# Kernel optimization log

Hardware: AMD Instinct MI355X
Metric: run time of the kernel (lower is better)

The kernel has to match this reference:

```python
import jax, jax.numpy as jnp
import numpy as np

B, DZ, DY, DX = 2, 200, 200, 100   # batch, voxel grid
N = 200000                          # active input voxels
C_IN, C_MID, C_OUT = 16, 64, 32
K = 27                              # 3x3x3 kernel offsets
EPS = 1e-5


def _pad_per_k(kid, a_in, a_out, pad_in, pad_out):
    # pack ragged per-offset pair lists into dense [K, Pmax] with dummy padding
    counts = np.bincount(kid, minlength=K)
    P = int(counts.max())
    I = np.full((K, P), pad_in, np.int32)
    O = np.full((K, P), pad_out, np.int32)
    order = np.argsort(kid, kind='stable')
    ks = kid[order]
    starts = np.cumsum(counts) - counts
    pos = np.arange(kid.size) - starts[ks]
    I[ks, pos] = a_in[order]
    O[ks, pos] = a_out[order]
    return I, O


def _build_structure(seed=0):
    # spconv-style indice-pair generation (rulebook) in numpy
    rng = np.random.default_rng(seed)
    lin = rng.choice(B * DZ * DY * DX, size=N, replace=False)
    b, r = np.divmod(lin, DZ * DY * DX)
    z, r = np.divmod(r, DY * DX)
    y, x = np.divmod(r, DX)
    coords = np.stack([b, z, y, x], 1)
    offs = np.stack(np.meshgrid(*[np.arange(3)] * 3, indexing='ij'), -1).reshape(K, 3)
    od = np.array([(DZ - 3) // 2 + 1, (DY - 3) // 2 + 1, (DX - 3) // 2 + 1])
    # stage 1: SparseConv3d k=3 s=2 p=0 -> output site o iff i = 2*o + k
    oc = coords[:, None, 1:] - offs[None]            # (N, 27, 3)
    valid = (oc >= 0).all(-1) & (oc % 2 == 0).all(-1)
    oq = oc // 2
    valid &= (oq < od).all(-1)
    pi, pk = np.nonzero(valid)
    oz, oy, ox = oq[pi, pk, 0], oq[pi, pk, 1], oq[pi, pk, 2]
    olin = ((coords[pi, 0] * od[0] + oz) * od[1] + oy) * od[2] + ox
    uniq, inv = np.unique(olin, return_inverse=True)
    n1 = int(len(uniq))
    p1_in, p1_out = _pad_per_k(pk, pi.astype(np.int32), inv.astype(np.int32), N, n1)
    # stage 2: SubMConv3d k=3 on stage-1 sites (output sites == input sites)
    c1b, r = np.divmod(uniq, od[0] * od[1] * od[2])
    c1z, r = np.divmod(r, od[1] * od[2])
    c1y, c1x = np.divmod(r, od[2])
    coords1 = np.stack([c1b, c1z, c1y, c1x], 1)
    nc = coords1[:, None, 1:] + (offs - 1)[None]     # (n1, 27, 3) neighbor coords
    valid2 = (nc >= 0).all(-1) & (nc < od).all(-1)
    pj, pk2 = np.nonzero(valid2)
    nl = ((coords1[pj, 0] * od[0] + nc[pj, pk2, 0]) * od[1] + nc[pj, pk2, 1]) * od[2] + nc[pj, pk2, 2]
    pos = np.minimum(np.searchsorted(uniq, nl), n1 - 1)
    ok = uniq[pos] == nl
    p2_in, p2_out = _pad_per_k(pk2[ok], pos[ok].astype(np.int32), pj[ok].astype(np.int32), n1, n1)
    return p1_in, p1_out, p2_in, p2_out, n1


def _ggs(feats, W, pin, pout, n_out):
    # gather-gemm-scatter sparse conv; pin padded with feats.shape[0], pout with n_out
    fpad = jnp.concatenate([feats, jnp.zeros((1, feats.shape[1]), feats.dtype)], 0)
    out = jnp.zeros((n_out + 1, W.shape[2]), feats.dtype)
    for k in range(W.shape[0]):
        out = out.at[pout[k]].add(fpad[pin[k]] @ W[k])
    return out[:n_out]


def _bn_relu(x, g, b):
    # BatchNorm1d (training-mode batch stats, biased var) + ReLU
    m = x.mean(0)
    v = x.var(0)
    return jax.nn.relu((x - m) * jax.lax.rsqrt(v + EPS) * g + b)


def setup_inputs():
    p1_in, p1_out, p2_in, p2_out, n1 = _build_structure(0)
    key = jax.random.key(0)
    k1, k2, k3, k4 = jax.random.split(key, 4)
    return {
        'feats': jax.random.normal(k1, (N, C_IN), jnp.float32),
        'W1': jax.random.normal(k2, (K, C_IN, C_MID), jnp.float32) * 0.05,
        'gamma1': jnp.ones((C_MID,), jnp.float32),
        'beta1': jnp.zeros((C_MID,), jnp.float32),
        'W2': jax.random.normal(k3, (K, C_MID, C_MID), jnp.float32) * 0.05,
        'gamma2': jnp.ones((C_MID,), jnp.float32),
        'beta2': jnp.zeros((C_MID,), jnp.float32),
        'W3': jax.random.normal(k4, (K, C_MID, C_OUT), jnp.float32) * 0.05,
        'p1_in': jnp.asarray(p1_in), 'p1_out': jnp.asarray(p1_out),
        'p2_in': jnp.asarray(p2_in), 'p2_out': jnp.asarray(p2_out),
        'n1': n1,
    }


def reference(feats, W1, gamma1, beta1, W2, gamma2, beta2, W3, p1_in, p1_out, p2_in, p2_out, n1):
    x = _ggs(feats, W1, p1_in, p1_out, n1)                        # SparseConv3d(Cin,64,3,2)
    x = _bn_relu(x, gamma1, beta1)
    x = _bn_relu(_ggs(x, W2, p2_in, p2_out, n1), gamma2, beta2)   # SubMConv3d(64,64,3)
    return _ggs(x, W3, p1_out, p1_in, N)                          # SparseInverseConv3d: pairs swapped
```

## Files before the change

kernel.cpp:

```cpp
#include <hip/hip_runtime.h>
#include <hip/hip_bf16.h>

typedef __bf16 bf16x8 __attribute__((ext_vector_type(8)));
typedef float f32x4 __attribute__((ext_vector_type(4)));

__device__ __forceinline__ unsigned short f2bf(float x) {
  union { float f; unsigned int u; } v; v.f = x;
  unsigned int r = (v.u + 0x7FFFu + ((v.u >> 16) & 1u)) >> 16;
  return (unsigned short)r;
}
__device__ __forceinline__ float bf2f(unsigned short u) {
  union { unsigned int u; float f; } v; v.u = ((unsigned int)u) << 16;
  return v.f;
}

__global__ void cvt_feats_kernel(const float* __restrict__ f, unsigned short* __restrict__ fb, int n16) {
  int t = blockIdx.x * 256 + threadIdx.x;
  if (t >= n16) return;
  int i = t >> 4, j = t & 15;
  fb[(size_t)i * 32 + j] = f2bf(f[t]);
}

__global__ void pack_w_kernel(const float* __restrict__ W, unsigned short* __restrict__ Wp,
                              int CI, int CO, int NT, int KK) {
  int t = blockIdx.x * 256 + threadIdx.x;
  int total = 27 * NT * KK * 512;
  if (t >= total) return;
  int j = t & 7, l = (t >> 3) & 63;
  int g = t >> 9;
  int kk = g % KK; g /= KK;
  int nt = g % NT; int k = g / NT;
  int kg = kk * 32 + ((l >> 4) * 8) + j;
  int c = nt * 16 + (l & 15);
  float v = (kg < CI) ? W[((size_t)k * CI + kg) * CO + c] : 0.0f;
  Wp[t] = f2bf(v);
}

__global__ void build_table_kernel(const int* __restrict__ pin, const int* __restrict__ pout,
                                   int P, int maxo, int* __restrict__ tab,
                                   const int* __restrict__ n_ptr, int n_cap) {
  int p = blockIdx.x * 256 + threadIdx.x;
  if (p >= P) return;
  int k = blockIdx.y;
  int n = n_cap;
  if (n_ptr) { int nv = n_ptr[0]; if (nv < n) n = nv; }
  size_t e = (size_t)k * P + p;
  int o = pout[e];
  if (o < n) tab[(size_t)k * maxo + o] = pin[e];
}

#define LDTAB(KC_, T0, T1) do {                                                  \
    int _kc = (KC_) > 26 ? 26 : (KC_);                                           \
    T0 = ok0 ? tab[(size_t)_kc * maxo + row0] : -1;                              \
    T1 = ok1 ? tab[(size_t)_kc * maxo + row1] : -1;                              \
  } while (0)

#define ISSUE_A(AB, T0, T1, D) do {                                              \
    if (SKIP) D = (__ballot((T0) >= 0 || (T1) >= 0) != 0ull);                    \
    const unsigned short* _s0 = Xb + (size_t)((T0) < 0 ? zrow : (T0)) * ROWS + lg * 8; \
    _Pragma("unroll") for (int kk = 0; kk < KK; ++kk)                            \
      AB[0][kk] = *reinterpret_cast<const bf16x8*>(_s0 + kk * 32);               \
    const unsigned short* _s1 = Xb + (size_t)((T1) < 0 ? zrow : (T1)) * ROWS + lg * 8; \
    _Pragma("unroll") for (int kk = 0; kk < KK; ++kk)                            \
      AB[1][kk] = *reinterpret_cast<const bf16x8*>(_s1 + kk * 32);               \
  } while (0)

#define STAGE_B(K, BUF) do {                                                     \
    if ((K) <= 26) {                                                             \
      size_t _kb = (size_t)(K) * (size_t)(KK * NT * 1024);                       \
      _Pragma("unroll") for (int _j = 0; _j < PER; ++_j) {                       \
        int _c = w * PER + _j;                                                   \
        const unsigned char* _gp = WpB + _kb + (size_t)_c * 1024 + (size_t)l * 16; \
        __builtin_amdgcn_global_load_lds(                                        \
            (const __attribute__((address_space(1))) void*)_gp,                  \
            (__attribute__((address_space(3))) void*)(&BUF[_c * 1024]), 16, 0, 0); \
      }                                                                          \
    }                                                                            \
  } while (0)

#define STEP_CORE(BCUR, AB, D) do {                                              \
    if (!SKIP || (D)) {                                                          \
      _Pragma("unroll") for (int kk = 0; kk < KK; ++kk)                          \
        _Pragma("unroll") for (int nt = 0; nt < NT; ++nt) {                      \
          bf16x8 b = *reinterpret_cast<const bf16x8*>(&(BCUR)[(nt * KK + kk) * 1024 + l * 16]); \
          acc[0][nt] = __builtin_amdgcn_mfma_f32_16x16x32_bf16(AB[0][kk], b, acc[0][nt], 0, 0, 0); \
          acc[1][nt] = __builtin_amdgcn_mfma_f32_16x16x32_bf16(AB[1][kk], b, acc[1][nt], 0, 0, 0); \
        }                                                                        \
    }                                                                            \
  } while (0)

template<int KK, int NT, bool SKIP>
__global__ __launch_bounds__(256, 3) void conv_mfma_kernel(
    const unsigned short* __restrict__ Xb, const unsigned short* __restrict__ Wp,
    const int* __restrict__ tab, int maxo, int zrow,
    const int* __restrict__ n_ptr, int n_cap,
    unsigned short* __restrict__ outb, float* __restrict__ outf) {
  const int CO = NT * 16;
  const int ROWS = KK * 32;
  constexpr int PER = (KK * NT) / 4;
  constexpr int SZ = KK * NT * 1024;

  __shared__ __align__(16) unsigned char Blds[3][SZ];

  int bid = blockIdx.x;
  {
    int nwg = gridDim.x;
    int q = nwg >> 3, r = nwg & 7;
    int xcd = bid & 7, orig = bid >> 3;
    bid = (xcd < r ? xcd * (q + 1) : r * (q + 1) + (xcd - r) * q) + orig;
  }

  int w = threadIdx.x >> 6, l = threadIdx.x & 63;
  int n_rows = n_cap;
  if (n_ptr) { int nv = n_ptr[0]; if (nv < n_rows) n_rows = nv; }
  if (bid * 128 >= n_rows) return;
  int lr = l & 15, lg = l >> 4;
  int wbase = bid * 128 + w * 32;
  int row0 = wbase + lr, row1 = wbase + 16 + lr;
  bool ok0 = row0 < n_rows, ok1 = row1 < n_rows;

  const unsigned char* WpB = (const unsigned char*)Wp;

  f32x4 acc[2][NT] = {};
  bf16x8 a0[2][KK], a1[2][KK];
  int tE0, tE1, tO0, tO1;
  bool dE = true, dO = true;

  LDTAB(0, tE0, tE1);
  LDTAB(1, tO0, tO1);
  STAGE_B(0, Blds[0]);
  STAGE_B(1, Blds[1]);
  ISSUE_A(a0, tE0, tE1, dE);
  ISSUE_A(a1, tO0, tO1, dO);
  LDTAB(2, tE0, tE1);
  LDTAB(3, tO0, tO1);
  __syncthreads();

  int cur = 0;
#pragma unroll 1
  for (int k = 0; k < 26; k += 2) {
    STAGE_B(k + 2, Blds[(cur + 2) % 3]);
    STEP_CORE(Blds[cur], a0, dE);
    ISSUE_A(a0, tE0, tE1, dE);
    LDTAB(k + 4, tE0, tE1);
    __syncthreads();
    STAGE_B(k + 3, Blds[cur]);
    STEP_CORE(Blds[(cur + 1) % 3], a1, dO);
    ISSUE_A(a1, tO0, tO1, dO);
    LDTAB(k + 5, tO0, tO1);
    __syncthreads();
    cur = (cur + 2) % 3;
  }
  STEP_CORE(Blds[cur], a0, dE);

#pragma unroll
  for (int mt = 0; mt < 2; ++mt) {
    int r0 = wbase + mt * 16 + lg * 4;
#pragma unroll
    for (int rr = 0; rr < 4; ++rr) {
      int row = r0 + rr;
      if (row < n_rows) {
#pragma unroll
        for (int nt = 0; nt < NT; ++nt) {
          size_t off = (size_t)row * CO + nt * 16 + lr;
          if (outf) outf[off] = acc[mt][nt][rr];
          else outb[off] = f2bf(acc[mt][nt][rr]);
        }
      }
    }
  }
}

__global__ void bn_stats_kernel(const unsigned short* __restrict__ xb,
                                const int* __restrict__ n_ptr, int n_cap,
                                float* __restrict__ stats) {
  int c = threadIdx.x & 63, q = threadIdx.x >> 6;
  int n = n_ptr[0]; if (n > n_cap) n = n_cap;
  float s = 0.f, ss = 0.f;
  for (int r = blockIdx.x * 4 + q; r < n; r += gridDim.x * 4) {
    float v = bf2f(xb[(size_t)r * 64 + c]);
    s += v; ss += v * v;
  }
  __shared__ float ls[8][64];
  ls[q][c] = s; ls[4 + q][c] = ss;
  __syncthreads();
  if (q == 0) {
    s = ls[0][c] + ls[1][c] + ls[2][c] + ls[3][c];
    ss = ls[4][c] + ls[5][c] + ls[6][c] + ls[7][c];
    atomicAdd(&stats[c], s);
    atomicAdd(&stats[64 + c], ss);
  }
}

__global__ void bn_apply_kernel(unsigned short* __restrict__ xb,
                                const int* __restrict__ n_ptr, int n_cap,
                                const float* __restrict__ stats,
                                const float* __restrict__ gamma, const float* __restrict__ beta) {
  int c = threadIdx.x & 63, q = threadIdx.x >> 6;
  int n = n_ptr[0]; if (n > n_cap) n = n_cap;
  float inv_n = 1.f / (float)n;
  float m = stats[c] * inv_n;
  float var = stats[64 + c] * inv_n - m * m;
  float sc = gamma[c] * rsqrtf(var + 1e-5f);
  float sh = beta[c] - m * sc;
  for (int r = blockIdx.x * 4 + q; r < n; r += gridDim.x * 4) {
    size_t off = (size_t)r * 64 + c;
    float v = bf2f(xb[off]) * sc + sh;
    xb[off] = f2bf(v > 0.f ? v : 0.f);
  }
}

extern "C" void kernel_launch(void* const* d_in, const int* in_sizes, int n_in,
                              void* d_out, int out_size, void* d_ws, size_t ws_size,
                              hipStream_t stream) {
  const float* feats  = (const float*)d_in[0];
  const float* W1     = (const float*)d_in[1];
  const float* g1     = (const float*)d_in[2];
  const float* b1     = (const float*)d_in[3];
  const float* W2     = (const float*)d_in[4];
  const float* g2     = (const float*)d_in[5];
  const float* b2     = (const float*)d_in[6];
  const float* W3     = (const float*)d_in[7];
  const int* p1_in    = (const int*)d_in[8];
  const int* p1_out   = (const int*)d_in[9];
  const int* p2_in    = (const int*)d_in[10];
  const int* p2_out   = (const int*)d_in[11];
  const int* d_n1     = (const int*)d_in[12];
  float* out = (float*)d_out;

  const int N  = in_sizes[0] / 16;
  const int P1 = in_sizes[8] / 27;
  const int P2 = in_sizes[10] / 27;
  long KP1 = in_sizes[8];
  int n1b = (int)(KP1 < 980100 ? KP1 : 980100);
  int maxo = n1b > N ? n1b : N;

  char* p = (char*)d_ws;
  auto alloc = [&](size_t bytes) -> char* {
    char* r = p; p += (bytes + 255) & ~(size_t)255; return r;
  };
  unsigned short* featsb = (unsigned short*)alloc((size_t)(N + 1) * 32 * 2);
  unsigned short* x1b    = (unsigned short*)alloc((size_t)(n1b + 1) * 64 * 2);
  unsigned short* x2b    = (unsigned short*)alloc((size_t)(n1b + 1) * 64 * 2);
  unsigned short* W1p    = (unsigned short*)alloc((size_t)27 * 4 * 1 * 512 * 2);
  unsigned short* W2p    = (unsigned short*)alloc((size_t)27 * 4 * 2 * 512 * 2);
  unsigned short* W3p    = (unsigned short*)alloc((size_t)27 * 2 * 2 * 512 * 2);
  int*   tab   = (int*)alloc((size_t)maxo * 27 * 4);
  float* stats = (float*)alloc(256 * 4);
  if ((size_t)(p - (char*)d_ws) > ws_size) return;

  hipMemsetAsync(featsb, 0, (size_t)(N + 1) * 32 * 2, stream);
  hipMemsetAsync(x1b + (size_t)n1b * 64, 0, 64 * 2, stream);
  hipMemsetAsync(x2b + (size_t)n1b * 64, 0, 64 * 2, stream);
  hipMemsetAsync(stats, 0, 256 * 4, stream);

  cvt_feats_kernel<<<(N * 16 + 255) / 256, 256, 0, stream>>>(feats, featsb, N * 16);
  pack_w_kernel<<<(27 * 4 * 1 * 512 + 255) / 256, 256, 0, stream>>>(W1, W1p, 16, 64, 4, 1);
  pack_w_kernel<<<(27 * 4 * 2 * 512 + 255) / 256, 256, 0, stream>>>(W2, W2p, 64, 64, 4, 2);
  pack_w_kernel<<<(27 * 2 * 2 * 512 + 255) / 256, 256, 0, stream>>>(W3, W3p, 64, 32, 2, 2);

  hipMemsetAsync(tab, 0xFF, (size_t)n1b * 27 * 4, stream);
  build_table_kernel<<<dim3((P1 + 255) / 256, 27), 256, 0, stream>>>(
      p1_in, p1_out, P1, n1b, tab, d_n1, n1b);
  conv_mfma_kernel<1, 4, true><<<(n1b + 127) / 128, 256, 0, stream>>>(
      featsb, W1p, tab, n1b, N, d_n1, n1b, x1b, nullptr);
  bn_stats_kernel<<<1024, 256, 0, stream>>>(x1b, d_n1, n1b, stats);
  bn_apply_kernel<<<2048, 256, 0, stream>>>(x1b, d_n1, n1b, stats, g1, b1);

  hipMemsetAsync(tab, 0xFF, (size_t)n1b * 27 * 4, stream);
  build_table_kernel<<<dim3((P2 + 255) / 256, 27), 256, 0, stream>>>(
      p2_in, p2_out, P2, n1b, tab, d_n1, n1b);
  conv_mfma_kernel<2, 4, false><<<(n1b + 127) / 128, 256, 0, stream>>>(
      x1b, W2p, tab, n1b, n1b, d_n1, n1b, x2b, nullptr);
  bn_stats_kernel<<<1024, 256, 0, stream>>>(x2b, d_n1, n1b, stats + 128);
  bn_apply_kernel<<<2048, 256, 0, stream>>>(x2b, d_n1, n1b, stats + 128, g2, b2);

  hipMemsetAsync(tab, 0xFF, (size_t)N * 27 * 4, stream);
  build_table_kernel<<<dim3((P1 + 255) / 256, 27), 256, 0, stream>>>(
      p1_out, p1_in, P1, N, tab, nullptr, N);
  conv_mfma_kernel<2, 2, true><<<(N + 127) / 128, 256, 0, stream>>>(
      x2b, W3p, tab, N, n1b, nullptr, N, nullptr, out);
}
```

Measured before the change: 671.5 us.

## Stage weight slices four offsets at a time with double-buffered LDS groups

Replaces the three-slot ring of per-offset weight buffers with two groups of four offset slices in LDS. Each group is prefetched with global_load_lds while the previous group is consumed, so barriers drop from one per offset to one per four offsets. The cost is a larger LDS footprint (eight slices instead of three), which can lower the number of resident workgroups per CU for the wider-channel convolutions.

```diff
diff --git a/kernel.cpp b/kernel.cpp
--- a/kernel.cpp
+++ b/kernel.cpp
@@ -65,15 +65,17 @@
       AB[1][kk] = *reinterpret_cast<const bf16x8*>(_s1 + kk * 32);               \
   } while (0)
 
-#define STAGE_B(K, BUF) do {                                                     \
-    if ((K) <= 26) {                                                             \
-      size_t _kb = (size_t)(K) * (size_t)(KK * NT * 1024);                       \
-      _Pragma("unroll") for (int _j = 0; _j < PER; ++_j) {                       \
-        int _c = w * PER + _j;                                                   \
-        const unsigned char* _gp = WpB + _kb + (size_t)_c * 1024 + (size_t)l * 16; \
-        __builtin_amdgcn_global_load_lds(                                        \
-            (const __attribute__((address_space(1))) void*)_gp,                  \
-            (__attribute__((address_space(3))) void*)(&BUF[_c * 1024]), 16, 0, 0); \
+#define STAGE_B4(KB, PB) do {                                                    \
+    _Pragma("unroll") for (int _s = 0; _s < 4; ++_s) {                           \
+      if ((KB) + _s <= 26) {                                                     \
+        size_t _kb = (size_t)((KB) + _s) * (size_t)SZ;                           \
+        _Pragma("unroll") for (int _j = 0; _j < PER; ++_j) {                     \
+          int _c = w * PER + _j;                                                 \
+          const unsigned char* _gp = WpB + _kb + (size_t)_c * 1024 + (size_t)l * 16; \
+          __builtin_amdgcn_global_load_lds(                                      \
+              (const __attribute__((address_space(1))) void*)_gp,                \
+              (__attribute__((address_space(3))) void*)((PB) + _s * SZ + _c * 1024), 16, 0, 0); \
+        }                                                                        \
       }                                                                          \
     }                                                                            \
   } while (0)
@@ -100,7 +102,7 @@
   constexpr int PER = (KK * NT) / 4;
   constexpr int SZ = KK * NT * 1024;
 
-  __shared__ __align__(16) unsigned char Blds[3][SZ];
+  __shared__ __align__(16) unsigned char Blds[2][4][SZ];
 
   int bid = blockIdx.x;
   {
@@ -128,30 +130,25 @@
 
   LDTAB(0, tE0, tE1);
   LDTAB(1, tO0, tO1);
-  STAGE_B(0, Blds[0]);
-  STAGE_B(1, Blds[1]);
+  STAGE_B4(0, &Blds[0][0][0]);
   ISSUE_A(a0, tE0, tE1, dE);
   ISSUE_A(a1, tO0, tO1, dO);
   LDTAB(2, tE0, tE1);
   LDTAB(3, tO0, tO1);
   __syncthreads();
 
-  int cur = 0;
 #pragma unroll 1
-  for (int k = 0; k < 26; k += 2) {
-    STAGE_B(k + 2, Blds[(cur + 2) % 3]);
-    STEP_CORE(Blds[cur], a0, dE);
-    ISSUE_A(a0, tE0, tE1, dE);
-    LDTAB(k + 4, tE0, tE1);
+  for (int g = 0; g < 7; ++g) {
+    int kb = g * 4;
+    unsigned char* bc = &Blds[g & 1][0][0];
+    unsigned char* bn = &Blds[(g + 1) & 1][0][0];
+    STAGE_B4(kb + 4, bn);
+    {           STEP_CORE(bc + 0 * SZ, a0, dE); ISSUE_A(a0, tE0, tE1, dE); LDTAB(kb + 4, tE0, tE1); }
+    {           STEP_CORE(bc + 1 * SZ, a1, dO); ISSUE_A(a1, tO0, tO1, dO); LDTAB(kb + 5, tO0, tO1); }
+    if (kb + 2 < 27) { STEP_CORE(bc + 2 * SZ, a0, dE); ISSUE_A(a0, tE0, tE1, dE); LDTAB(kb + 6, tE0, tE1); }
+    if (kb + 3 < 27) { STEP_CORE(bc + 3 * SZ, a1, dO); ISSUE_A(a1, tO0, tO1, dO); LDTAB(kb + 7, tO0, tO1); }
     __syncthreads();
-    STAGE_B(k + 3, Blds[cur]);
-    STEP_CORE(Blds[(cur + 1) % 3], a1, dO);
-    ISSUE_A(a1, tO0, tO1, dO);
-    LDTAB(k + 5, tO0, tO1);
-    __syncthreads();
-    cur = (cur + 2) % 3;
-  }
-  STEP_CORE(Blds[cur], a0, dE);
+  }
 
 #pragma unroll
   for (int mt = 0; mt < 2; ++mt) {
```

After: 714.3 us. +6.4%, slower.
